# Performance work log

Hardware: AMD Instinct MI355X
Metric: run time of the kernel (lower is better)

Reference implementation:

```python
import jax, jax.numpy as jnp
import numpy as np

CHUNK = 128  # chunk size for the causal linear-attention recurrence
EPS = 1e-10


def _causal_numerator(q, k, v, chunk=CHUNK):
    """N_i = sum_{j<=i} (q_i . k_j) v_j, computed chunk-recurrently.

    q,k: [B,H,N,D]; v: [B,H,N,E] -> [B,H,N,E]
    """
    B, H, N, D = q.shape
    E = v.shape[-1]
    nc = N // chunk
    qc = jnp.moveaxis(q.reshape(B, H, nc, chunk, D), 2, 0)  # [nc,B,H,c,D]
    kc = jnp.moveaxis(k.reshape(B, H, nc, chunk, D), 2, 0)
    vc = jnp.moveaxis(v.reshape(B, H, nc, chunk, E), 2, 0)
    mask = jnp.tril(jnp.ones((chunk, chunk), dtype=q.dtype))  # causal within chunk

    def step(S, inp):  # S: running sum of k_j (outer) v_j -> [B,H,D,E]
        qi, ki, vi = inp
        scores = jnp.einsum('bhid,bhjd->bhij', qi, ki) * mask
        intra = jnp.einsum('bhij,bhje->bhie', scores, vi)
        inter = jnp.einsum('bhid,bhde->bhie', qi, S)
        S = S + jnp.einsum('bhjd,bhje->bhde', ki, vi)
        return S, intra + inter

    S0 = jnp.zeros((B, H, D, E), q.dtype)
    _, outs = jax.lax.scan(step, S0, (qc, kc, vc))  # [nc,B,H,c,E]
    return jnp.moveaxis(outs, 0, 2).reshape(B, H, N, E)


def _causal_denominator(q, k):
    # D_i = q_i . cumsum_j<=i k_j  -> [B,H,N]
    return jnp.einsum('bhnd,bhnd->bhn', q, jnp.cumsum(k, axis=-2))


def setup_inputs() -> dict:
    key = jax.random.key(0)
    ks = jax.random.split(key, 5)
    shape = (2, 8, 4096, 64)
    names = ['q', 'k', 'q_rot', 'k_rot', 'v']
    # feature-mapped inputs (Performer softmax features) are positive
    return {n: jax.random.uniform(ks[i], shape, dtype=jnp.float32) for i, n in enumerate(names)}


def reference(q, k, q_rot, k_rot, v):
    N = _causal_numerator(q, k, v) + _causal_numerator(q_rot, k_rot, v)
    D = _causal_denominator(q, k) + _causal_denominator(q_rot, k_rot)
    return N * (1.0 / (D + EPS))[..., None]
```

## Files before the change

kernel.cpp:

```cpp
#include <hip/hip_runtime.h>

#define SEQ 4096
#define DIM 64
#define CHUNK 128
#define NC 32
#define EPSV 1e-10f
#define KS_OFF 2097152

typedef __attribute__((ext_vector_type(8))) short s16x8;
typedef __attribute__((ext_vector_type(4))) float f32x4;

__device__ __forceinline__ unsigned short f2bf(float f) {
  unsigned int u = __float_as_uint(f);
  u += 0x7FFF + ((u >> 16) & 1);
  return (unsigned short)(u >> 16);
}

__device__ __forceinline__ unsigned int cvtpk(float lo, float hi) {
  unsigned int r;
  asm("v_cvt_pk_bf16_f32 %0, %1, %2" : "=v"(r) : "v"(lo), "v"(hi));
  return r;
}
__device__ __forceinline__ s16x8 pack8(float4 a, float4 b) {
  union { unsigned int u[4]; s16x8 v; } r;
  r.u[0] = cvtpk(a.x, a.y); r.u[1] = cvtpk(a.z, a.w);
  r.u[2] = cvtpk(b.x, b.y); r.u[3] = cvtpk(b.z, b.w);
  return r.v;
}

__device__ __forceinline__ int swz512(int b) { return ((b & 7) << 6) | (b >> 3); }

template<bool SUM, int TPB>
__device__ __forceinline__ float gather_T(const float* __restrict__ gp,
                                          unsigned short* __restrict__ dst, int t) {
  int d = t & 63, grp = t >> 6;
  constexpr int GRPS = TPB / 64;
  constexpr int NI = 16 / GRPS;
  float s = 0.f;
#pragma unroll
  for (int i = 0; i < NI; ++i) {
    int j8 = grp + i * GRPS;
    const float* p = gp + (size_t)(j8 * 8) * DIM + d;
    float x[8];
#pragma unroll
    for (int u2 = 0; u2 < 8; ++u2) x[u2] = p[(size_t)u2 * DIM];
    if (SUM) {
#pragma unroll
      for (int u2 = 0; u2 < 8; ++u2) s += x[u2];
    }
    union { unsigned int u4[4]; s16x8 v; } seg;
#pragma unroll
    for (int u2 = 0; u2 < 4; ++u2) seg.u4[u2] = cvtpk(x[2 * u2], x[2 * u2 + 1]);
    *(s16x8*)&dst[d * 136 + j8 * 8] = seg.v;
  }
  return s;
}

__global__ __launch_bounds__(512, 4) void pass_a(const float* __restrict__ k0,
                                                 const float* __restrict__ k1,
                                                 const float* __restrict__ v,
                                                 float* __restrict__ ws) {
  __shared__ __align__(16) unsigned short skT[2][64 * 136];
  __shared__ __align__(16) unsigned short svT[64 * 136];
  __shared__ float spart[2][4][64];
  int bid = swz512(blockIdx.x);
  int hh = bid >> 5, c = bid & 31;
  int t = threadIdx.x, half = t >> 8, tt = t & 255;
  size_t off = (size_t)hh * SEQ * DIM + (size_t)c * CHUNK * DIM;
  const float* kp = (half ? k1 : k0) + off;
  int chunk = half * 512 + hh * 32 + c;

  float s = gather_T<true, 256>(kp, skT[half], tt);
  gather_T<false, 512>(v + off, svT, t);
  spart[half][tt >> 6][tt & 63] = s;
  __syncthreads();

  if (tt < 64)
    ws[KS_OFF + (size_t)chunk * 64 + tt] = spart[half][0][tt] + spart[half][1][tt]
                                         + spart[half][2][tt] + spart[half][3][tt];

  int wv = tt >> 6, L = tt & 63, g = L >> 4, cL = L & 15;
  f32x4 acc[4];
#pragma unroll
  for (int ct = 0; ct < 4; ++ct) acc[ct] = (f32x4){0.f, 0.f, 0.f, 0.f};
#pragma unroll
  for (int ks = 0; ks < 4; ++ks) {
    s16x8 aF = *(const s16x8*)&svT[(wv * 16 + cL) * 136 + ks * 32 + g * 8];
#pragma unroll
    for (int ct = 0; ct < 4; ++ct) {
      s16x8 bF = *(const s16x8*)&skT[half][(ct * 16 + cL) * 136 + ks * 32 + g * 8];
      acc[ct] = __builtin_amdgcn_mfma_f32_16x16x32_bf16(aF, bF, acc[ct], 0, 0, 0);
    }
  }
  unsigned short* Sp = (unsigned short*)ws + (size_t)chunk * 4096;
#pragma unroll
  for (int ct = 0; ct < 4; ++ct)
#pragma unroll
    for (int r = 0; r < 4; ++r)
      Sp[(size_t)(wv * 16 + g * 4 + r) * 64 + ct * 16 + cL] = f2bf(acc[ct][r]);
}

__global__ __launch_bounds__(512, 4) void pass_c(const float* __restrict__ q0,
                                                 const float* __restrict__ q1,
                                                 const float* __restrict__ k0,
                                                 const float* __restrict__ k1,
                                                 const float* __restrict__ v,
                                                 const float* __restrict__ ws,
                                                 float* __restrict__ out) {
  __shared__ __align__(16) unsigned short svT[64 * 136];
  __shared__ __align__(16) union UBuf {
    struct {
      unsigned short sST[2][64 * 72];
      float skpref[2][64];
    } a;
    float exch[128 * 66];
  } u;
  __shared__ float sden[2][128];

  int bid = swz512(blockIdx.x);
  int hh = bid >> 5, c = bid & 31;
  int t = threadIdx.x;
  int w = t >> 6, L = t & 63, g = L >> 4, cL = L & 15;
  int half = t >> 8, tt = t & 255;
  size_t off = (size_t)hh * SEQ * DIM + (size_t)c * CHUNK * DIM;
  const int rtS0 = w, rtS1 = 7 - w;

  gather_T<false, 512>(v + off, svT, t);

  {
    int cb = half * 512 + hh * 32;
    const unsigned int* S32 = (const unsigned int*)ws;
    float aS[16];
#pragma unroll
    for (int i = 0; i < 16; ++i) aS[i] = 0.f;
    for (int cc = 0; cc < c; ++cc) {
      const unsigned int* p = S32 + (size_t)(cb + cc) * 2048 + tt * 8;
      uint4 A = *(const uint4*)p;
      uint4 B = *(const uint4*)(p + 4);
      aS[0]  += __uint_as_float(A.x << 16); aS[1]  += __uint_as_float(A.x & 0xFFFF0000u);
      aS[2]  += __uint_as_float(A.y << 16); aS[3]  += __uint_as_float(A.y & 0xFFFF0000u);
      aS[4]  += __uint_as_float(A.z << 16); aS[5]  += __uint_as_float(A.z & 0xFFFF0000u);
      aS[6]  += __uint_as_float(A.w << 16); aS[7]  += __uint_as_float(A.w & 0xFFFF0000u);
      aS[8]  += __uint_as_float(B.x << 16); aS[9]  += __uint_as_float(B.x & 0xFFFF0000u);
      aS[10] += __uint_as_float(B.y << 16); aS[11] += __uint_as_float(B.y & 0xFFFF0000u);
      aS[12] += __uint_as_float(B.z << 16); aS[13] += __uint_as_float(B.z & 0xFFFF0000u);
      aS[14] += __uint_as_float(B.w << 16); aS[15] += __uint_as_float(B.w & 0xFFFF0000u);
    }
    union { unsigned int u4[4]; s16x8 v8; } w0, w1;
#pragma unroll
    for (int i = 0; i < 4; ++i) w0.u4[i] = cvtpk(aS[2 * i], aS[2 * i + 1]);
#pragma unroll
    for (int i = 0; i < 4; ++i) w1.u4[i] = cvtpk(aS[8 + 2 * i], aS[8 + 2 * i + 1]);
    int i0 = 2 * tt, i1 = 2 * tt + 1;
    *(s16x8*)&u.a.sST[half][(i0 >> 3) * 72 + (i0 & 7) * 8] = w0.v8;
    *(s16x8*)&u.a.sST[half][(i1 >> 3) * 72 + (i1 & 7) * 8] = w1.v8;
    if (tt < 64) {
      float run = 0.f;
      for (int cc = 0; cc < c; ++cc) run += ws[KS_OFF + (size_t)(cb + cc) * 64 + tt];
      u.a.skpref[half][tt] = run;
    }
  }
  __syncthreads();

  f32x4 accO[2][4];
#pragma unroll
  for (int a = 0; a < 2; ++a)
#pragma unroll
    for (int b = 0; b < 4; ++b) accO[a][b] = (f32x4){0.f, 0.f, 0.f, 0.f};
  float dent[2] = {0.f, 0.f};
  s16x8 aq[2][2];

#pragma unroll
  for (int s2 = 0; s2 < 2; ++s2) {
    int rt = s2 ? rtS1 : rtS0;
    const float* qp = (s2 ? q1 : q0) + off;
    int row = rt * 16 + cL;
#pragma unroll
    for (int h = 0; h < 2; ++h) {
      const float* qb = qp + (size_t)row * DIM + h * 32 + g * 8;
      float4 a0 = *(const float4*)qb;
      float4 a1 = *(const float4*)(qb + 4);
      const float* kq = &u.a.skpref[s2][h * 32 + g * 8];
      dent[s2] += a0.x * kq[0] + a0.y * kq[1] + a0.z * kq[2] + a0.w * kq[3]
                + a1.x * kq[4] + a1.y * kq[5] + a1.z * kq[6] + a1.w * kq[7];
      aq[s2][h] = pack8(a0, a1);
    }
#pragma unroll
    for (int h = 0; h < 2; ++h)
#pragma unroll
      for (int et = 0; et < 4; ++et) {
        s16x8 bS = *(const s16x8*)&u.a.sST[s2][(et * 16 + cL) * 72 + h * 32 + g * 8];
        accO[s2][et] = __builtin_amdgcn_mfma_f32_16x16x32_bf16(aq[s2][h], bS, accO[s2][et], 0, 0, 0);
      }
  }

  {
    int srcA = cL + ((g & 1) << 5), srcB = srcA + 16;
    bool hiG = g >= 2;
#pragma unroll
    for (int s2 = 0; s2 < 2; ++s2) {
      int rt = s2 ? rtS1 : rtS0;
      const float* kp = (s2 ? k1 : k0) + off;
      for (int ks = 0; ks <= (rt >> 1); ++ks) {
        unsigned int E0e, E1e;
        {
          int jt = 2 * ks;
          const float* kb = kp + (size_t)(jt * 16 + cL) * DIM;
          float4 b0 = *(const float4*)(kb + g * 8);
          float4 b1 = *(const float4*)(kb + g * 8 + 4);
          float4 b2 = *(const float4*)(kb + 32 + g * 8);
          float4 b3 = *(const float4*)(kb + 32 + g * 8 + 4);
          s16x8 kf0 = pack8(b0, b1), kf1 = pack8(b2, b3);
          f32x4 C = (f32x4){0.f, 0.f, 0.f, 0.f};
          C = __builtin_amdgcn_mfma_f32_16x16x32_bf16(kf0, aq[s2][0], C, 0, 0, 0);
          C = __builtin_amdgcn_mfma_f32_16x16x32_bf16(kf1, aq[s2][1], C, 0, 0, 0);
          if (jt == rt) {
#pragma unroll
            for (int r = 0; r < 4; ++r)
              if (g * 4 + r > cL) C[r] = 0.f;
          }
          dent[s2] += C[0] + C[1] + C[2] + C[3];
          E0e = cvtpk(C[0], C[1]); E1e = cvtpk(C[2], C[3]);
        }
        int S0o = 0, S1o = 0, S2o = 0, S3o = 0;
        if (2 * ks + 1 <= rt) {
          int jt = 2 * ks + 1;
          const float* kb = kp + (size_t)(jt * 16 + cL) * DIM;
          float4 b0 = *(const float4*)(kb + g * 8);
          float4 b1 = *(const float4*)(kb + g * 8 + 4);
          float4 b2 = *(const float4*)(kb + 32 + g * 8);
          float4 b3 = *(const float4*)(kb + 32 + g * 8 + 4);
          s16x8 kf0 = pack8(b0, b1), kf1 = pack8(b2, b3);
          f32x4 C = (f32x4){0.f, 0.f, 0.f, 0.f};
          C = __builtin_amdgcn_mfma_f32_16x16x32_bf16(kf0, aq[s2][0], C, 0, 0, 0);
          C = __builtin_amdgcn_mfma_f32_16x16x32_bf16(kf1, aq[s2][1], C, 0, 0, 0);
          if (jt == rt) {
#pragma unroll
            for (int r = 0; r < 4; ++r)
              if (g * 4 + r > cL) C[r] = 0.f;
          }
          dent[s2] += C[0] + C[1] + C[2] + C[3];
          unsigned int E0o = cvtpk(C[0], C[1]), E1o = cvtpk(C[2], C[3]);
          S0o = __shfl((int)E0o, srcA); S1o = __shfl((int)E1o, srcA);
          S2o = __shfl((int)E0o, srcB); S3o = __shfl((int)E1o, srcB);
        }
        int S0e = __shfl((int)E0e, srcA); int S1e = __shfl((int)E1e, srcA);
        int S2e = __shfl((int)E0e, srcB); int S3e = __shfl((int)E1e, srcB);
        union { int d4[4]; s16x8 v8; } ap;
        ap.d4[0] = hiG ? S0o : S0e;
        ap.d4[1] = hiG ? S1o : S1e;
        ap.d4[2] = hiG ? S2o : S2e;
        ap.d4[3] = hiG ? S3o : S3e;
#pragma unroll
        for (int et = 0; et < 4; ++et) {
          s16x8 bV = *(const s16x8*)&svT[(et * 16 + cL) * 136 + ks * 32 + g * 8];
          accO[s2][et] = __builtin_amdgcn_mfma_f32_16x16x32_bf16(ap.v8, bV, accO[s2][et], 0, 0, 0);
        }
      }
    }
  }

#pragma unroll
  for (int s2 = 0; s2 < 2; ++s2) {
    float dt = dent[s2];
    dt += __shfl_xor(dt, 16);
    dt += __shfl_xor(dt, 32);
    dent[s2] = dt;
  }
  if (L < 16) {
    sden[0][rtS0 * 16 + L] = dent[0];
    sden[1][rtS1 * 16 + L] = dent[1];
  }
  __syncthreads();

#pragma unroll
  for (int et = 0; et < 4; ++et)
#pragma unroll
    for (int r = 0; r < 4; ++r)
      u.exch[(rtS1 * 16 + g * 4 + r) * 66 + et * 16 + cL] = accO[1][et][r];
  __syncthreads();

  float* op = out + off;
#pragma unroll
  for (int r = 0; r < 4; ++r) {
    int row = rtS0 * 16 + g * 4 + r;
    float inv = 1.f / (sden[0][row] + sden[1][row] + EPSV);
#pragma unroll
    for (int et = 0; et < 4; ++et) {
      float O = accO[0][et][r] + u.exch[row * 66 + et * 16 + cL];
      op[(size_t)row * DIM + et * 16 + cL] = O * inv;
    }
  }
}

extern "C" void kernel_launch(void* const* d_in, const int* in_sizes, int n_in,
                              void* d_out, int out_size, void* d_ws, size_t ws_size,
                              hipStream_t stream) {
  const float* q  = (const float*)d_in[0];
  const float* k  = (const float*)d_in[1];
  const float* qr = (const float*)d_in[2];
  const float* kr = (const float*)d_in[3];
  const float* v  = (const float*)d_in[4];
  float* out = (float*)d_out;
  float* ws  = (float*)d_ws;

  hipLaunchKernelGGL(pass_a, dim3(512), dim3(512), 0, stream, k, kr, v, ws);
  hipLaunchKernelGGL(pass_c, dim3(512), dim3(512), 0, stream, q, qr, k, kr, v, ws, out);
}
```

Before: 151.3 us.

## Fuse chunk-state and output kernels using per-chunk ready flags

Merges the two passes into one kernel. Each block computes its chunk's k^T v state and k-sum, publishes a release flag, then spins until all earlier chunks of the same head have published before reducing the prefix. This removes one kernel launch boundary and reuses the transposed V tile already held in LDS, so V is no longer gathered twice. In exchange it adds a memset launch, agent-scope atomic loads, and a spin-wait whose progress depends on the earlier blocks being resident or already finished.

```diff
diff --git a/kernel.cpp b/kernel.cpp
--- a/kernel.cpp
+++ b/kernel.cpp
@@ -6,6 +6,7 @@
 #define NC 32
 #define EPSV 1e-10f
 #define KS_OFF 2097152
+#define FLAG_OFF (KS_OFF + 65536)
 
 typedef __attribute__((ext_vector_type(8))) short s16x8;
 typedef __attribute__((ext_vector_type(4))) float f32x4;
@@ -29,6 +30,20 @@
 }
 
 __device__ __forceinline__ int swz512(int b) { return ((b & 7) << 6) | (b >> 3); }
+
+__device__ __forceinline__ void flag_store(float* p) {
+  __hip_atomic_store((unsigned int*)p, 1u, __ATOMIC_RELEASE, __HIP_MEMORY_SCOPE_AGENT);
+}
+__device__ __forceinline__ unsigned int flag_load(const float* p) {
+  return __hip_atomic_load((const unsigned int*)p, __ATOMIC_RELAXED, __HIP_MEMORY_SCOPE_AGENT);
+}
+__device__ __forceinline__ unsigned long long ld64_agent(const unsigned long long* p) {
+  return __hip_atomic_load(p, __ATOMIC_RELAXED, __HIP_MEMORY_SCOPE_AGENT);
+}
+__device__ __forceinline__ float ldf_agent(const float* p) {
+  unsigned int x = __hip_atomic_load((const unsigned int*)p, __ATOMIC_RELAXED, __HIP_MEMORY_SCOPE_AGENT);
+  return __uint_as_float(x);
+}
 
 template<bool SUM, int TPB>
 __device__ __forceinline__ float gather_T(const float* __restrict__ gp,
@@ -56,95 +71,92 @@
   return s;
 }
 
-__global__ __launch_bounds__(512, 4) void pass_a(const float* __restrict__ k0,
-                                                 const float* __restrict__ k1,
-                                                 const float* __restrict__ v,
-                                                 float* __restrict__ ws) {
-  __shared__ __align__(16) unsigned short skT[2][64 * 136];
+__global__ __launch_bounds__(512, 4) void fused(const float* __restrict__ q0,
+                                                const float* __restrict__ q1,
+                                                const float* __restrict__ k0,
+                                                const float* __restrict__ k1,
+                                                const float* __restrict__ v,
+                                                float* __restrict__ ws,
+                                                float* __restrict__ out) {
   __shared__ __align__(16) unsigned short svT[64 * 136];
-  __shared__ float spart[2][4][64];
+  __shared__ float sden[2][128];
+  __shared__ __align__(16) union UB {
+    struct { unsigned short skT[2][64 * 136]; float spart[2][4][64]; } a;
+    struct { unsigned short sST[2][64 * 72]; float skpref[2][64]; } c1;
+    float exch[128 * 66];
+  } u;
+
   int bid = swz512(blockIdx.x);
   int hh = bid >> 5, c = bid & 31;
   int t = threadIdx.x, half = t >> 8, tt = t & 255;
   size_t off = (size_t)hh * SEQ * DIM + (size_t)c * CHUNK * DIM;
+  int chunk = half * 512 + hh * 32 + c;
+  float* flags = ws + FLAG_OFF + (size_t)hh * 32;
+
   const float* kp = (half ? k1 : k0) + off;
-  int chunk = half * 512 + hh * 32 + c;
-
-  float s = gather_T<true, 256>(kp, skT[half], tt);
+  float s = gather_T<true, 256>(kp, u.a.skT[half], tt);
   gather_T<false, 512>(v + off, svT, t);
-  spart[half][tt >> 6][tt & 63] = s;
+  u.a.spart[half][tt >> 6][tt & 63] = s;
   __syncthreads();
 
   if (tt < 64)
-    ws[KS_OFF + (size_t)chunk * 64 + tt] = spart[half][0][tt] + spart[half][1][tt]
-                                         + spart[half][2][tt] + spart[half][3][tt];
-
-  int wv = tt >> 6, L = tt & 63, g = L >> 4, cL = L & 15;
-  f32x4 acc[4];
-#pragma unroll
-  for (int ct = 0; ct < 4; ++ct) acc[ct] = (f32x4){0.f, 0.f, 0.f, 0.f};
-#pragma unroll
-  for (int ks = 0; ks < 4; ++ks) {
-    s16x8 aF = *(const s16x8*)&svT[(wv * 16 + cL) * 136 + ks * 32 + g * 8];
-#pragma unroll
-    for (int ct = 0; ct < 4; ++ct) {
-      s16x8 bF = *(const s16x8*)&skT[half][(ct * 16 + cL) * 136 + ks * 32 + g * 8];
-      acc[ct] = __builtin_amdgcn_mfma_f32_16x16x32_bf16(aF, bF, acc[ct], 0, 0, 0);
-    }
-  }
-  unsigned short* Sp = (unsigned short*)ws + (size_t)chunk * 4096;
-#pragma unroll
-  for (int ct = 0; ct < 4; ++ct)
-#pragma unroll
-    for (int r = 0; r < 4; ++r)
-      Sp[(size_t)(wv * 16 + g * 4 + r) * 64 + ct * 16 + cL] = f2bf(acc[ct][r]);
-}
-
-__global__ __launch_bounds__(512, 4) void pass_c(const float* __restrict__ q0,
-                                                 const float* __restrict__ q1,
-                                                 const float* __restrict__ k0,
-                                                 const float* __restrict__ k1,
-                                                 const float* __restrict__ v,
-                                                 const float* __restrict__ ws,
-                                                 float* __restrict__ out) {
-  __shared__ __align__(16) unsigned short svT[64 * 136];
-  __shared__ __align__(16) union UBuf {
-    struct {
-      unsigned short sST[2][64 * 72];
-      float skpref[2][64];
-    } a;
-    float exch[128 * 66];
-  } u;
-  __shared__ float sden[2][128];
-
-  int bid = swz512(blockIdx.x);
-  int hh = bid >> 5, c = bid & 31;
-  int t = threadIdx.x;
+    ws[KS_OFF + (size_t)chunk * 64 + tt] = u.a.spart[half][0][tt] + u.a.spart[half][1][tt]
+                                         + u.a.spart[half][2][tt] + u.a.spart[half][3][tt];
+
+  {
+    int wv = tt >> 6, Lp = tt & 63, gp2 = Lp >> 4, cLp = Lp & 15;
+    f32x4 acc[4];
+#pragma unroll
+    for (int ct = 0; ct < 4; ++ct) acc[ct] = (f32x4){0.f, 0.f, 0.f, 0.f};
+#pragma unroll
+    for (int ks = 0; ks < 4; ++ks) {
+      s16x8 aF = *(const s16x8*)&svT[(wv * 16 + cLp) * 136 + ks * 32 + gp2 * 8];
+#pragma unroll
+      for (int ct = 0; ct < 4; ++ct) {
+        s16x8 bF = *(const s16x8*)&u.a.skT[half][(ct * 16 + cLp) * 136 + ks * 32 + gp2 * 8];
+        acc[ct] = __builtin_amdgcn_mfma_f32_16x16x32_bf16(aF, bF, acc[ct], 0, 0, 0);
+      }
+    }
+    unsigned short* Sp = (unsigned short*)ws + (size_t)chunk * 4096;
+#pragma unroll
+    for (int ct = 0; ct < 4; ++ct)
+#pragma unroll
+      for (int r = 0; r < 4; ++r)
+        Sp[(size_t)(wv * 16 + gp2 * 4 + r) * 64 + ct * 16 + cLp] = f2bf(acc[ct][r]);
+  }
+
+  __syncthreads();
+  if (t == 0) {
+    __threadfence();
+    flag_store(&flags[c]);
+  }
+
   int w = t >> 6, L = t & 63, g = L >> 4, cL = L & 15;
-  int half = t >> 8, tt = t & 255;
-  size_t off = (size_t)hh * SEQ * DIM + (size_t)c * CHUNK * DIM;
   const int rtS0 = w, rtS1 = 7 - w;
 
-  gather_T<false, 512>(v + off, svT, t);
-
+  if (c > 0) {
+    if (w == 0 && L < c) {
+      while (flag_load(&flags[L]) == 0u) __builtin_amdgcn_s_sleep(2);
+    }
+    __syncthreads();
+  }
   {
     int cb = half * 512 + hh * 32;
-    const unsigned int* S32 = (const unsigned int*)ws;
+    const unsigned long long* S64 = (const unsigned long long*)ws;
     float aS[16];
 #pragma unroll
     for (int i = 0; i < 16; ++i) aS[i] = 0.f;
     for (int cc = 0; cc < c; ++cc) {
-      const unsigned int* p = S32 + (size_t)(cb + cc) * 2048 + tt * 8;
-      uint4 A = *(const uint4*)p;
-      uint4 B = *(const uint4*)(p + 4);
-      aS[0]  += __uint_as_float(A.x << 16); aS[1]  += __uint_as_float(A.x & 0xFFFF0000u);
-      aS[2]  += __uint_as_float(A.y << 16); aS[3]  += __uint_as_float(A.y & 0xFFFF0000u);
-      aS[4]  += __uint_as_float(A.z << 16); aS[5]  += __uint_as_float(A.z & 0xFFFF0000u);
-      aS[6]  += __uint_as_float(A.w << 16); aS[7]  += __uint_as_float(A.w & 0xFFFF0000u);
-      aS[8]  += __uint_as_float(B.x << 16); aS[9]  += __uint_as_float(B.x & 0xFFFF0000u);
-      aS[10] += __uint_as_float(B.y << 16); aS[11] += __uint_as_float(B.y & 0xFFFF0000u);
-      aS[12] += __uint_as_float(B.z << 16); aS[13] += __uint_as_float(B.z & 0xFFFF0000u);
-      aS[14] += __uint_as_float(B.w << 16); aS[15] += __uint_as_float(B.w & 0xFFFF0000u);
+      const unsigned long long* p = S64 + (size_t)(cb + cc) * 1024 + tt * 4;
+#pragma unroll
+      for (int qd = 0; qd < 4; ++qd) {
+        unsigned long long q = ld64_agent(p + qd);
+        unsigned int d0 = (unsigned int)q, d1 = (unsigned int)(q >> 32);
+        aS[4 * qd + 0] += __uint_as_float(d0 << 16);
+        aS[4 * qd + 1] += __uint_as_float(d0 & 0xFFFF0000u);
+        aS[4 * qd + 2] += __uint_as_float(d1 << 16);
+        aS[4 * qd + 3] += __uint_as_float(d1 & 0xFFFF0000u);
+      }
     }
     union { unsigned int u4[4]; s16x8 v8; } w0, w1;
 #pragma unroll
@@ -152,12 +164,13 @@
 #pragma unroll
     for (int i = 0; i < 4; ++i) w1.u4[i] = cvtpk(aS[8 + 2 * i], aS[8 + 2 * i + 1]);
     int i0 = 2 * tt, i1 = 2 * tt + 1;
-    *(s16x8*)&u.a.sST[half][(i0 >> 3) * 72 + (i0 & 7) * 8] = w0.v8;
-    *(s16x8*)&u.a.sST[half][(i1 >> 3) * 72 + (i1 & 7) * 8] = w1.v8;
+    *(s16x8*)&u.c1.sST[half][(i0 >> 3) * 72 + (i0 & 7) * 8] = w0.v8;
+    *(s16x8*)&u.c1.sST[half][(i1 >> 3) * 72 + (i1 & 7) * 8] = w1.v8;
     if (tt < 64) {
       float run = 0.f;
-      for (int cc = 0; cc < c; ++cc) run += ws[KS_OFF + (size_t)(cb + cc) * 64 + tt];
-      u.a.skpref[half][tt] = run;
+      for (int cc = 0; cc < c; ++cc)
+        run += ldf_agent(&ws[KS_OFF + (size_t)(cb + cc) * 64 + tt]);
+      u.c1.skpref[half][tt] = run;
     }
   }
   __syncthreads();
@@ -180,7 +193,7 @@
       const float* qb = qp + (size_t)row * DIM + h * 32 + g * 8;
       float4 a0 = *(const float4*)qb;
       float4 a1 = *(const float4*)(qb + 4);
-      const float* kq = &u.a.skpref[s2][h * 32 + g * 8];
+      const float* kq = &u.c1.skpref[s2][h * 32 + g * 8];
       dent[s2] += a0.x * kq[0] + a0.y * kq[1] + a0.z * kq[2] + a0.w * kq[3]
                 + a1.x * kq[4] + a1.y * kq[5] + a1.z * kq[6] + a1.w * kq[7];
       aq[s2][h] = pack8(a0, a1);
@@ -189,7 +202,7 @@
     for (int h = 0; h < 2; ++h)
 #pragma unroll
       for (int et = 0; et < 4; ++et) {
-        s16x8 bS = *(const s16x8*)&u.a.sST[s2][(et * 16 + cL) * 72 + h * 32 + g * 8];
+        s16x8 bS = *(const s16x8*)&u.c1.sST[s2][(et * 16 + cL) * 72 + h * 32 + g * 8];
         accO[s2][et] = __builtin_amdgcn_mfma_f32_16x16x32_bf16(aq[s2][h], bS, accO[s2][et], 0, 0, 0);
       }
   }
@@ -200,12 +213,12 @@
 #pragma unroll
     for (int s2 = 0; s2 < 2; ++s2) {
       int rt = s2 ? rtS1 : rtS0;
-      const float* kp = (s2 ? k1 : k0) + off;
+      const float* kpp = (s2 ? k1 : k0) + off;
       for (int ks = 0; ks <= (rt >> 1); ++ks) {
         unsigned int E0e, E1e;
         {
           int jt = 2 * ks;
-          const float* kb = kp + (size_t)(jt * 16 + cL) * DIM;
+          const float* kb = kpp + (size_t)(jt * 16 + cL) * DIM;
           float4 b0 = *(const float4*)(kb + g * 8);
           float4 b1 = *(const float4*)(kb + g * 8 + 4);
           float4 b2 = *(const float4*)(kb + 32 + g * 8);
@@ -225,7 +238,7 @@
         int S0o = 0, S1o = 0, S2o = 0, S3o = 0;
         if (2 * ks + 1 <= rt) {
           int jt = 2 * ks + 1;
-          const float* kb = kp + (size_t)(jt * 16 + cL) * DIM;
+          const float* kb = kpp + (size_t)(jt * 16 + cL) * DIM;
           float4 b0 = *(const float4*)(kb + g * 8);
           float4 b1 = *(const float4*)(kb + g * 8 + 4);
           float4 b2 = *(const float4*)(kb + 32 + g * 8);
@@ -304,6 +317,6 @@
   float* out = (float*)d_out;
   float* ws  = (float*)d_ws;
 
-  hipLaunchKernelGGL(pass_a, dim3(512), dim3(512), 0, stream, k, kr, v, ws);
-  hipLaunchKernelGGL(pass_c, dim3(512), dim3(512), 0, stream, q, qr, k, kr, v, ws, out);
-}
+  hipMemsetAsync(ws + FLAG_OFF, 0, 512 * sizeof(float), stream);
+  hipLaunchKernelGGL(fused, dim3(512), dim3(512), 0, stream, q, qr, k, kr, v, ws, out);
+}
```

Result: slower. 206.3 us (+36.3%).
